# Optimization experiments

Measured on AMD Instinct MI355X. Metric: run time of the kernel, lower is better.

## Reference

```python
import jax, jax.numpy as jnp
import numpy as np

B = 65536
DIM = 8
HIS_LEN = 5
KIND_LEN = 10
HIS_ITEM_DIM = (1 + KIND_LEN) * DIM  # 88
ALL_DIM = DIM * (5 + KIND_LEN) + HIS_ITEM_DIM  # 208


def _linear_params(key, in_dim, out_dim):
    k1, k2 = jax.random.split(key)
    bound = 1.0 / np.sqrt(in_dim)
    w = jax.random.uniform(k1, (out_dim, in_dim), jnp.float32, -bound, bound)
    b = jax.random.uniform(k2, (out_dim,), jnp.float32, -bound, bound)
    return w, b


def setup_inputs() -> dict:
    key = jax.random.key(0)
    ks = jax.random.split(key, 20)
    inp = {
        'userid': jax.random.randint(ks[0], (B, 1), 0, 1000000),
        'itemid': jax.random.randint(ks[1], (B, 1), 0, 1000000),
        'user_age': jax.random.randint(ks[2], (B, 1), 0, 8),
        'gender': jax.random.randint(ks[3], (B, 1), 0, 3),
        'user_occupation': jax.random.randint(ks[4], (B, 1), 0, 25),
        'item_kind': jax.random.randint(ks[5], (B, KIND_LEN), 0, 20),
        'item_id_his': jax.random.randint(ks[6], (B, HIS_LEN), 0, 1000000),
        'item_kind_his': jax.random.randint(ks[7], (B, HIS_LEN, KIND_LEN), 0, 20),
        'user_emb': jax.random.normal(ks[8], (1000000, DIM), jnp.float32),
        'item_emb': jax.random.normal(ks[9], (1000000, DIM), jnp.float32),
        'age_emb': jax.random.normal(ks[10], (8, DIM), jnp.float32),
        'gender_emb': jax.random.normal(ks[11], (3, DIM), jnp.float32),
        'occ_emb': jax.random.normal(ks[12], (25, DIM), jnp.float32),
        'kind_emb': jax.random.normal(ks[13], (20, DIM), jnp.float32),
    }
    act_dims = [(HIS_ITEM_DIM * 3, 64), (64, 32), (32, 1)]
    for i, (di, do) in enumerate(act_dims, 1):
        w, b = _linear_params(jax.random.fold_in(key, 100 + i), di, do)
        inp[f'act_w{i}'], inp[f'act_b{i}'] = w, b
    mlp_dims = [(ALL_DIM, 128), (128, 64), (64, 32), (32, 1)]
    for i, (di, do) in enumerate(mlp_dims, 1):
        w, b = _linear_params(jax.random.fold_in(key, 200 + i), di, do)
        inp[f'mlp_w{i}'], inp[f'mlp_b{i}'] = w, b
    return inp


def _forward(userid, itemid, user_age, gender, user_occupation, item_kind,
             item_id_his, item_kind_his, user_emb, item_emb, age_emb,
             gender_emb, occ_emb, kind_emb,
             act_w1, act_b1, act_w2, act_b2, act_w3, act_b3,
             mlp_w1, mlp_b1, mlp_w2, mlp_b2, mlp_w3, mlp_b3, mlp_w4, mlp_b4):
    b = userid.shape[0]
    user_w = user_emb[userid]          # [b,1,8]
    item_w = item_emb[itemid]          # [b,1,8]
    age_w = age_emb[user_age]          # [b,1,8]
    gen_w = gender_emb[gender]         # [b,1,8]
    occ_w = occ_emb[user_occupation]   # [b,1,8]
    kind_w = kind_emb[item_kind]       # [b,10,8]
    kind_w = kind_w * (item_kind != 0)[..., None].astype(kind_w.dtype)

    # history: vectorized over his_len
    his_item_w = item_emb[item_id_his]           # [b,5,8]
    his_kind_w = kind_emb[item_kind_his]         # [b,5,10,8]
    his_kind_w = his_kind_w * (item_kind_his != 0)[..., None].astype(his_kind_w.dtype)
    his_feature = jnp.concatenate([his_item_w[:, :, None, :], his_kind_w], axis=2)
    his_feature = his_feature.reshape(b, HIS_LEN, HIS_ITEM_DIM)  # [b,5,88]

    item_feat_now = jnp.concatenate([item_w, kind_w], axis=1).reshape(b, 1, HIS_ITEM_DIM)
    item_feat_now = jnp.broadcast_to(item_feat_now, (b, HIS_LEN, HIS_ITEM_DIM))

    # ActUnit: i_in = [i1, i1-i2, i2]; score = MLP(i_in); act_weight = i1 * score
    i1, i2 = his_feature, item_feat_now
    i_in = jnp.concatenate([i1, i1 - i2, i2], axis=-1)  # [b,5,264]
    h = jax.nn.relu(jnp.einsum('bsd,od->bso', i_in, act_w1) + act_b1)
    h = jax.nn.relu(jnp.einsum('bsd,od->bso', h, act_w2) + act_b2)
    score = jnp.einsum('bsd,od->bso', h, act_w3) + act_b3  # [b,5,1]
    act_weight = i1 * score
    his_pool = jnp.sum(his_feature * act_weight, axis=1)  # [b,88]

    all_feat = jnp.concatenate([user_w, item_w, age_w, gen_w, occ_w, kind_w], axis=1).reshape(b, -1)
    all_feat = jnp.concatenate([all_feat, his_pool], axis=-1)  # [b,208]

    h = jax.nn.relu(all_feat @ mlp_w1.T + mlp_b1)
    h = jax.nn.relu(h @ mlp_w2.T + mlp_b2)
    h = jax.nn.relu(h @ mlp_w3.T + mlp_b3)
    logit = h @ mlp_w4.T + mlp_b4  # [b,1]
    return jax.nn.sigmoid(logit)


def reference(userid, itemid, user_age, gender, user_occupation, item_kind,
              item_id_his, item_kind_his, user_emb, item_emb, age_emb,
              gender_emb, occ_emb, kind_emb,
              act_w1, act_b1, act_w2, act_b2, act_w3, act_b3,
              mlp_w1, mlp_b1, mlp_w2, mlp_b2, mlp_w3, mlp_b3, mlp_w4, mlp_b4):
    return _forward(userid, itemid, user_age, gender, user_occupation, item_kind,
                    item_id_his, item_kind_his, user_emb, item_emb, age_emb,
                    gender_emb, occ_emb, kind_emb,
                    act_w1, act_b1, act_w2, act_b2, act_w3, act_b3,
                    mlp_w1, mlp_b1, mlp_w2, mlp_b2, mlp_w3, mlp_b3, mlp_w4, mlp_b4)
```

## Files before the change

### kernel.cpp

```cpp
#include <hip/hip_runtime.h>
#include <cstdint>
#include <math.h>

#define BATCH    65536
#define HIS_LEN  5
#define KIND_LEN 10
#define SB       64
#define NTH      256

typedef float    v2f __attribute__((ext_vector_type(2)));
typedef float    v4f __attribute__((ext_vector_type(4)));
typedef _Float16 v2h __attribute__((ext_vector_type(2)));
typedef _Float16 v8h __attribute__((ext_vector_type(8)));
__device__ __forceinline__ v2f mk2(float a, float b){ v2f r; r.x=a; r.y=b; return r; }
#define C2H(u)  __builtin_bit_cast(v2h,(unsigned)(u))
#define C8H(u4) __builtin_bit_cast(v8h,(u4))

#if __has_builtin(__builtin_amdgcn_fdot2)
__device__ __forceinline__ float FD2(v2h a, v2h b, float c){
  return __builtin_amdgcn_fdot2(a, b, c, false);
}
#else
__device__ __forceinline__ float FD2(v2h a, v2h b, float c){
  return c + (float)a.x*(float)b.x + (float)a.y*(float)b.y;
}
#endif

__device__ __forceinline__ unsigned short f2h(float f){
  return __builtin_bit_cast(unsigned short, (_Float16)f);
}
__device__ __forceinline__ unsigned pack2h(float a, float b){
  return (unsigned)f2h(a) | ((unsigned)f2h(b) << 16);
}
__device__ __forceinline__ v2h pkh(float a, float b){
  return __builtin_bit_cast(v2h, __builtin_amdgcn_cvt_pkrtz(a, b));
}

#define OFF_WC1H 0
#define OFF_AB1  6144
#define OFF_W2H  6208
#define OFF_AB2  7232
#define OFF_W3   7264
#define OFF_AB3  7296
#define OFF_MB2  7297
#define OFF_MB3  7361
#define OFF_M4   7393
#define OFF_MB4  7425
#define OFF_M3H  7428
#define OFF_W1F  8452
#define OFF_MB1  22788
#define OFF_W2F  22916
#define PREP_N   27012
#define W1F4  2113
#define W2F4  5729
#define M3H4  1857

#define TPF   6144
#define M3HL  1856
#define PFF   8704
#define W2HF4 2192
#define MB1F  9986
#define H2F4  1088
#define LDSF  10114

typedef const float* fp;

__device__ __forceinline__ float m1s_val(fp m1, int o, int q, int t){
  if(t >= 52) return 0.f;
  int src;
  if(t<8){ int E = (q==0)?0:(8+8*q); src = E + t; }
  else if(t<30){ int d=t-8; int idx = 8*(d>>1)+2*q+(d&1);
                 src = (idx<8) ? (8+idx) : (32+idx); }
  else { int d=t-30; int idx = 8*(d>>1)+2*q+(d&1); src = 120+idx; }
  return m1[o*208 + src];
}
__device__ __forceinline__ float m1k(fp m1, int o, int k){
  return m1s_val(m1, o, k/56, k%56);
}
__device__ __forceinline__ float w1c_val(fp aw1, int o, int q, int h, int d){
  if(d >= 22) return 0.f;
  int idx = 8*(d>>1) + 2*q + (d&1);
  return h ? (aw1[o*264+176+idx] - aw1[o*264+88+idx])
           : (aw1[o*264+idx]     + aw1[o*264+88+idx]);
}

__global__ void din_prep(fp aw1, fp ab1, fp aw2, fp ab2, fp aw3, fp ab3,
                         fp m1,  fp mb1, fp m2,  fp mb2, fp m3,  fp mb3,
                         fp m4,  fp mb4, float* __restrict__ ws){
  int j = blockIdx.x*blockDim.x + threadIdx.x;
  unsigned* wsu = (unsigned*)ws;
  if(j < 6144){
    int h = j/3072, r = j%3072;
    int slot = r/12, dw = r - slot*12;
    int o = slot>>2, q = slot&3;
    wsu[OFF_WC1H + j] = pack2h(w1c_val(aw1,o,q,h,2*dw), w1c_val(aw1,o,q,h,2*dw+1));
    return;
  } j -= 6144;
  if(j < 64){ ws[OFF_AB1 + j] = ab1[j]; return; } j -= 64;
  if(j < 1024){
    int pp = j>>5, q = (j>>3)&3, dw = j&7;
    int o = 8*q + dw;
    wsu[OFF_W2H + j] = pack2h(aw2[o*64 + 2*pp], aw2[o*64 + 2*pp+1]);
    return;
  } j -= 1024;
  if(j < 32){ ws[OFF_AB2 + j] = ab2[j]; return; } j -= 32;
  if(j < 32){ ws[OFF_W3  + j] = aw3[j]; return; } j -= 32;
  if(j < 1){ ws[OFF_AB3] = ab3[0]; return; } j -= 1;
  if(j < 64){ ws[OFF_MB2 + j] = mb2[j]; return; } j -= 64;
  if(j < 32){ ws[OFF_MB3 + j] = mb3[j]; return; } j -= 32;
  if(j < 32){ ws[OFF_M4  + j] = m4[j];  return; } j -= 32;
  if(j < 1){ ws[OFF_MB4] = mb4[0]; return; } j -= 1;
  if(j < 2){ ws[7426 + j] = 0.f; return; } j -= 2;
  if(j < 1024){
    int qq = j>>8, rr = j&255, ip = rr>>5, dw = rr&31;
    wsu[OFF_M3H + j] = pack2h(m3[dw*64 + 16*qq + 2*ip], m3[dw*64 + 16*qq + 2*ip+1]);
    return;
  } j -= 1024;
  if(j < 14336){
    int frag = j>>2, jr = j&3;
    int lane = frag & 63, nt = frag >> 6;
    int n = nt/7, t = nt - 7*n;
    int o = 16*n + (lane&15);
    int k0 = t*32 + ((lane>>4)<<3) + 2*jr;
    wsu[OFF_W1F + j] = pack2h(m1k(m1,o,k0), m1k(m1,o,k0+1));
    return;
  } j -= 14336;
  if(j < 128){ ws[OFF_MB1 + j] = mb1[j]; return; } j -= 128;
  if(j < 4096){
    int frag = j>>2, jr = j&3;
    int lane = frag & 63, nt = frag >> 6;
    int n2 = nt>>2, t2 = nt&3;
    int o = 16*n2 + (lane&15);
    int k0 = t2*32 + ((lane>>4)<<3) + 2*jr;
    wsu[OFF_W2F + j] = pack2h(m2[o*128 + k0], m2[o*128 + k0+1]);
    return;
  }
}

template<int CTL>
__device__ __forceinline__ float qp(float v){
  return __uint_as_float((unsigned)__builtin_amdgcn_update_dpp(
      0, (int)__float_as_uint(v), CTL, 0xF, 0xF, true));
}
__device__ __forceinline__ float bsum4(float v){
  v += qp<0xB1>(v);
  v += qp<0x4E>(v);
  return v;
}

__device__ __forceinline__ void ldst16(void* l, const void* g){
  __builtin_amdgcn_global_load_lds(
      (const __attribute__((address_space(1))) unsigned int*)(uintptr_t)g,
      (__attribute__((address_space(3))) unsigned int*)(uintptr_t)l, 16, 0, 0);
}
__device__ __forceinline__ void ldst4(void* l, const void* g){
  __builtin_amdgcn_global_load_lds(
      (const __attribute__((address_space(1))) unsigned int*)(uintptr_t)g,
      (__attribute__((address_space(3))) unsigned int*)(uintptr_t)l, 4, 0, 0);
}

__device__ __forceinline__ void gather_h(const float2* __restrict__ itemp,
                                         const float2* __restrict__ kindp,
                                         int item_idx, const int* __restrict__ kidx,
                                         int q, v2h* f){
  float2 v = itemp[item_idx*4 + q];
  f[0] = pkh(v.x, v.y);
  #pragma unroll
  for(int r=0;r<KIND_LEN;r++){
    int ki = kidx[r];
    float2 w = kindp[ki*4 + q];
    float mx = ki ? w.x : 0.f, my = ki ? w.y : 0.f;
    f[1+r] = pkh(mx, my);
  }
}

template<int NS>
__device__ __forceinline__ void hist_pass(int b, int s0, int q, int wid,
    const float2* __restrict__ item_emb, const float2* __restrict__ kind_emb,
    const int* __restrict__ his_id, const int* __restrict__ his_kind,
    const float* ls, const float4* ls4, const unsigned* tpu, v2f* poolv){
  v2h i1h[NS][11];
  #pragma unroll
  for(int t=0;t<NS;t++)
    gather_h(item_emb, kind_emb, his_id[b*HIS_LEN + s0 + t],
             his_kind + (b*HIS_LEN + s0 + t)*KIND_LEN, q, i1h[t]);
  float h2s[NS][8];
  #pragma unroll
  for(int t=0;t<NS;t++)
    #pragma unroll
    for(int k=0;k<8;k++) h2s[t][k] = 0.f;

  #pragma unroll 1
  for(int p=0;p<32;p++){
    const uint4* wr0 = (const uint4*)(ls4 + ((2*p  )*4+q)*3);
    const uint4* wr1 = (const uint4*)(ls4 + ((2*p+1)*4+q)*3);
    uint4 r0=wr0[0], r1=wr0[1], r2=wr0[2];
    uint4 s0v=wr1[0], s1v=wr1[1], s2v=wr1[2];
    unsigned w0[12] = {r0.x,r0.y,r0.z,r0.w, r1.x,r1.y,r1.z,r1.w, r2.x,r2.y,r2.z,r2.w};
    unsigned w1[12] = {s0v.x,s0v.y,s0v.z,s0v.w, s1v.x,s1v.y,s1v.z,s1v.w, s2v.x,s2v.y,s2v.z,s2v.w};
    v2h t2 = C2H(tpu[p*SB + wid]);
    v2h hpv[NS];
    #pragma unroll
    for(int t=0;t<NS;t++){
      float aA=0.f, aB=0.f, cA=0.f, cB=0.f;
      #pragma unroll
      for(int u=0;u<11;u++){
        if(u&1){ aB = FD2(C2H(w0[u]), i1h[t][u], aB); cB = FD2(C2H(w1[u]), i1h[t][u], cB); }
        else   { aA = FD2(C2H(w0[u]), i1h[t][u], aA); cA = FD2(C2H(w1[u]), i1h[t][u], cA); }
      }
      float h0 = fmaxf(bsum4(aA+aB) + (float)t2.x, 0.f);
      float h1 = fmaxf(bsum4(cA+cB) + (float)t2.y, 0.f);
      hpv[t] = pkh(h0, h1);
    }
    uint4 wa = *(const uint4*)(ls4 + W2HF4 + (p*4+q)*2);
    uint4 wb = *(const uint4*)(ls4 + W2HF4 + (p*4+q)*2 + 1);
    unsigned w2d[8] = {wa.x,wa.y,wa.z,wa.w, wb.x,wb.y,wb.z,wb.w};
    #pragma unroll
    for(int t=0;t<NS;t++)
      #pragma unroll
      for(int k=0;k<8;k++) h2s[t][k] = FD2(C2H(w2d[k]), hpv[t], h2s[t][k]);
  }
  #pragma unroll
  for(int t=0;t<NS;t++){
    float scp = 0.f;
    #pragma unroll
    for(int j=0;j<8;j++){
      float hx = fmaxf(h2s[t][j] + ls[PFF+1088+8*q+j], 0.f);
      scp += ls[PFF+1120+8*q+j]*hx;
    }
    float sc = bsum4(scp) + ls[PFF+1152];
    #pragma unroll
    for(int j=0;j<11;j++){
      float sx = (float)i1h[t][j].x, sy = (float)i1h[t][j].y;
      poolv[j] = __builtin_elementwise_fma(mk2(sx*sc, sy*sc), mk2(sx, sy), poolv[j]);
    }
  }
}

__global__ void __launch_bounds__(NTH, 4)
din_main(const int* __restrict__ userid, const int* __restrict__ itemid,
         const int* __restrict__ age,    const int* __restrict__ gen,
         const int* __restrict__ occ,    const int* __restrict__ item_kind,
         const int* __restrict__ his_id, const int* __restrict__ his_kind,
         const float2* __restrict__ user_emb, const float2* __restrict__ item_emb,
         const float2* __restrict__ age_emb,  const float2* __restrict__ gen_emb,
         const float2* __restrict__ occ_emb,  const float2* __restrict__ kind_emb,
         const float* __restrict__ ws, float* __restrict__ out){
  const int tid  = threadIdx.x;
  const int q    = tid & 3;
  const int sl   = (tid & 63) >> 2;
  const int wv   = __builtin_amdgcn_readfirstlane(tid >> 6);
  const int wid  = wv*16 + sl;
  const int b    = blockIdx.x*SB + wid;
  const int l    = tid & 63;
  const int sA   = wv*16 + (l&15);
  const int kb   = l >> 4;

  __shared__ __align__(16) float ls[LDSF];
  float4* ls4 = (float4*)ls;
  const float* wsc = ws;
  const float4* ws4 = (const float4*)ws;
  const uint4* wsu4 = (const uint4*)ws;
  unsigned* tpu = (unsigned*)(ls + TPF);

  #pragma unroll
  for(int k=0;k<5;k++){ int j = k*NTH + tid; ldst4(ls + PFF + j, wsc + OFF_AB1 + j); }
  { int j = 5*NTH + tid;
    if(j < 1282) ldst4(ls + PFF + j, wsc + OFF_AB1 + j); }
  if(tid < 128) ldst4(ls + MB1F + tid, wsc + OFF_MB1 + tid);
  #pragma unroll
  for(int k=0;k<6;k++){ int j = k*NTH + tid; ldst16(ls4 + j, ws4 + j); }

  v2h i2h[11];
  gather_h(item_emb, kind_emb, itemid[b], item_kind + b*KIND_LEN, q, i2h);

  __syncthreads();

  #pragma unroll 1
  for(int p=0;p<32;p++){
    const uint4* wr0 = (const uint4*)(ls4 + 768 + ((2*p  )*4+q)*3);
    const uint4* wr1 = (const uint4*)(ls4 + 768 + ((2*p+1)*4+q)*3);
    uint4 r0=wr0[0], r1=wr0[1], r2=wr0[2];
    uint4 s0v=wr1[0], s1v=wr1[1], s2v=wr1[2];
    unsigned w0[12] = {r0.x,r0.y,r0.z,r0.w, r1.x,r1.y,r1.z,r1.w, r2.x,r2.y,r2.z,r2.w};
    unsigned w1[12] = {s0v.x,s0v.y,s0v.z,s0v.w, s1v.x,s1v.y,s1v.z,s1v.w, s2v.x,s2v.y,s2v.z,s2v.w};
    float aA=0.f, aB=0.f, cA=0.f, cB=0.f;
    #pragma unroll
    for(int u=0;u<11;u++){
      if(u&1){ aB = FD2(C2H(w0[u]), i2h[u], aB); cB = FD2(C2H(w1[u]), i2h[u], cB); }
      else   { aA = FD2(C2H(w0[u]), i2h[u], aA); cA = FD2(C2H(w1[u]), i2h[u], cA); }
    }
    float sA2 = bsum4(aA+aB), sB2 = bsum4(cA+cB);
    if(q==0){
      float2 bb = ((const float2*)(ls+PFF))[p];
      tpu[p*SB + wid] = __builtin_bit_cast(unsigned, pkh(sA2+bb.x, sB2+bb.y));
    }
  }
  __syncthreads();

  v2f poolv[11];
  #pragma unroll
  for(int d=0;d<11;d++) poolv[d]=mk2(0.f,0.f);
  hist_pass<2>(b, 0, q, wid, item_emb, kind_emb, his_id, his_kind, ls, ls4, tpu, poolv);
  hist_pass<2>(b, 2, q, wid, item_emb, kind_emb, his_id, his_kind, ls, ls4, tpu, poolv);
  hist_pass<1>(b, 4, q, wid, item_emb, kind_emb, his_id, his_kind, ls, ls4, tpu, poolv);

  gather_h(item_emb, kind_emb, itemid[b], item_kind + b*KIND_LEN, q, i2h);
  v2h fe[26];
  {
    const float2* ep = (q==0)? user_emb : (q==1)? age_emb : (q==2)? gen_emb : occ_emb;
    int ei = (q==0)? userid[b] : (q==1)? age[b] : (q==2)? gen[b] : occ[b];
    #pragma unroll
    for(int k=0;k<4;k++){ float2 v = ep[ei*4+k]; fe[k] = pkh(v.x, v.y); }
  }
  #pragma unroll
  for(int j=0;j<11;j++) fe[4+j]  = i2h[j];
  #pragma unroll
  for(int j=0;j<11;j++) fe[15+j] = pkh(poolv[j].x, poolv[j].y);

  __syncthreads();

  {
    unsigned xd[28];
    #pragma unroll
    for(int u=0;u<26;u++) xd[u] = __builtin_bit_cast(unsigned, fe[u]);
    xd[26] = 0; xd[27] = 0;
    uint4* xp = (uint4*)(ls4 + wid*29 + q*7);
    #pragma unroll
    for(int ct=0; ct<7; ct++){
      uint4 t; t.x=xd[4*ct]; t.y=xd[4*ct+1]; t.z=xd[4*ct+2]; t.w=xd[4*ct+3];
      xp[ct] = t;
    }
  }
  __syncthreads();

  uint4 af[7];
  #pragma unroll
  for(int t=0;t<7;t++) af[t] = *(const uint4*)(ls4 + sA*29 + t*4 + kb);

  ldst16(ls4 + M3HL + (tid>>6)*66 + (tid&63), ws4 + M3H4 + tid);

  __syncthreads();

  v4f acc1[8];
  #pragma unroll
  for(int n=0;n<8;n++){
    float bb = ls[MB1F + n*16 + (l&15)];
    v4f c = {bb, bb, bb, bb};
    #pragma unroll
    for(int t=0;t<7;t++){
      uint4 bw = wsu4[W1F4 + (n*7+t)*64 + l];
      c = __builtin_amdgcn_mfma_f32_16x16x32_f16(C8H(af[t]), C8H(bw), c, 0, 0, 0);
    }
    acc1[n] = c;
  }
  {
    _Float16* h1p = (_Float16*)ls;
    #pragma unroll
    for(int n=0;n<8;n++)
      #pragma unroll
      for(int i=0;i<4;i++)
        h1p[(wv*16 + kb*4 + i)*136 + 16*n + (l&15)] =
            (_Float16)fmaxf(acc1[n][i], 0.f);
  }
  __syncthreads();

  v4f acc2[4];
  #pragma unroll
  for(int n2=0;n2<4;n2++){
    float bb = ls[PFF+1153 + n2*16 + (l&15)];
    v4f c = {bb, bb, bb, bb};
    acc2[n2] = c;
  }
  #pragma unroll
  for(int t2=0;t2<4;t2++){
    uint4 aw = *(const uint4*)(ls4 + sA*17 + t2*4 + kb);
    #pragma unroll
    for(int n2=0;n2<4;n2++){
      uint4 bw = wsu4[W2F4 + (n2*4+t2)*64 + l];
      acc2[n2] = __builtin_amdgcn_mfma_f32_16x16x32_f16(C8H(aw), C8H(bw), acc2[n2], 0, 0, 0);
    }
  }
  {
    _Float16* h2p = (_Float16*)(ls4 + H2F4);
    #pragma unroll
    for(int n2=0;n2<4;n2++)
      #pragma unroll
      for(int i=0;i<4;i++)
        h2p[(wv*16 + kb*4 + i)*72 + 16*n2 + (l&15)] =
            (_Float16)fmaxf(acc2[n2][i], 0.f);
  }
  __syncthreads();

  v2h hp3[8];
  {
    const uint4* hr = (const uint4*)(ls4 + H2F4 + wid*9 + 2*q);
    uint4 d0 = hr[0], d1 = hr[1];
    hp3[0]=C2H(d0.x); hp3[1]=C2H(d0.y); hp3[2]=C2H(d0.z); hp3[3]=C2H(d0.w);
    hp3[4]=C2H(d1.x); hp3[5]=C2H(d1.y); hp3[6]=C2H(d1.z); hp3[7]=C2H(d1.w);
  }
  float x = ls[PFF+1281];
  #pragma unroll
  for(int g=0;g<4;g++){
    float a[8];
    #pragma unroll
    for(int j=0;j<8;j++) a[j]=0.f;
    #pragma unroll
    for(int ip=0;ip<8;ip++){
      const uint4* w3p = (const uint4*)(ls4 + M3HL + q*66 + ip*8 + 2*g);
      uint4 b0=w3p[0], b1=w3p[1];
      a[0]=FD2(C2H(b0.x),hp3[ip],a[0]); a[1]=FD2(C2H(b0.y),hp3[ip],a[1]);
      a[2]=FD2(C2H(b0.z),hp3[ip],a[2]); a[3]=FD2(C2H(b0.w),hp3[ip],a[3]);
      a[4]=FD2(C2H(b1.x),hp3[ip],a[4]); a[5]=FD2(C2H(b1.y),hp3[ip],a[5]);
      a[6]=FD2(C2H(b1.z),hp3[ip],a[6]); a[7]=FD2(C2H(b1.w),hp3[ip],a[7]);
    }
    #pragma unroll
    for(int j=0;j<8;j++) a[j] = bsum4(a[j]);
    #pragma unroll
    for(int j=0;j<8;j++)
      x += ls[PFF+1249+8*g+j] * fmaxf(a[j] + ls[PFF+1217+8*g+j], 0.f);
  }

  if(q==0) out[b] = 1.0f/(1.0f + __expf(-x));
}

extern "C" void kernel_launch(void* const* d_in, const int* in_sizes, int n_in,
                              void* d_out, int out_size, void* d_ws, size_t ws_size,
                              hipStream_t stream){
  const int* userid    = (const int*)d_in[0];
  const int* itemid    = (const int*)d_in[1];
  const int* age       = (const int*)d_in[2];
  const int* gen       = (const int*)d_in[3];
  const int* occ       = (const int*)d_in[4];
  const int* item_kind = (const int*)d_in[5];
  const int* his_id    = (const int*)d_in[6];
  const int* his_kind  = (const int*)d_in[7];
  const float2* user_emb = (const float2*)d_in[8];
  const float2* item_emb = (const float2*)d_in[9];
  const float2* age_emb  = (const float2*)d_in[10];
  const float2* gen_emb  = (const float2*)d_in[11];
  const float2* occ_emb  = (const float2*)d_in[12];
  const float2* kind_emb = (const float2*)d_in[13];
  float* ws = (float*)d_ws;

  din_prep<<<(PREP_N+255)/256, 256, 0, stream>>>(
      (fp)d_in[14], (fp)d_in[15], (fp)d_in[16], (fp)d_in[17], (fp)d_in[18], (fp)d_in[19],
      (fp)d_in[20], (fp)d_in[21], (fp)d_in[22], (fp)d_in[23], (fp)d_in[24], (fp)d_in[25],
      (fp)d_in[26], (fp)d_in[27], ws);

  din_main<<<BATCH/SB, NTH, 0, stream>>>(
      userid, itemid, age, gen, occ, item_kind, his_id, his_kind,
      user_emb, item_emb, age_emb, gen_emb, occ_emb, kind_emb,
      ws, (float*)d_out);
}
```

Baseline: 242.2 us.

## Compute attention MLP with MFMA per history step, prefetching next gather

Replaces the fdot2-based attention MLP (a per-sample target projection pass plus hist_pass loops over history items) with per-history-step MFMA matmuls. Each step feeds the concatenated history and target features into a 16x16x32 f16 MFMA for layer 1 and another MFMA for layer 2, then does a scalar layer 3 and accumulates the pooled result. The next history item's embedding gather is issued before the current step's matmuls so memory latency overlaps compute. The extra LDS this needs forces the launch-bounds occupancy hint down from 4 to 3 blocks, and each step adds three block barriers.

```diff
diff --git a/kernel.cpp b/kernel.cpp
--- a/kernel.cpp
+++ b/kernel.cpp
@@ -36,32 +36,34 @@
   return __builtin_bit_cast(v2h, __builtin_amdgcn_cvt_pkrtz(a, b));
 }
 
-#define OFF_WC1H 0
-#define OFF_AB1  6144
-#define OFF_W2H  6208
-#define OFF_AB2  7232
-#define OFF_W3   7264
-#define OFF_AB3  7296
-#define OFF_MB2  7297
-#define OFF_MB3  7361
-#define OFF_M4   7393
-#define OFF_MB4  7425
+#define OFF_HW1F 0
+#define OFF_AW2F 6144
+#define OFF_PF   7168
 #define OFF_M3H  7428
-#define OFF_W1F  8452
+#define OFF_MW1F 8452
 #define OFF_MB1  22788
-#define OFF_W2F  22916
+#define OFF_MW2F 22916
 #define PREP_N   27012
-#define W1F4  2113
-#define W2F4  5729
+#define AW2F4 1536
 #define M3H4  1857
-
-#define TPF   6144
-#define M3HL  1856
-#define PFF   8704
-#define W2HF4 2192
-#define MB1F  9986
-#define H2F4  1088
-#define LDSF  10114
+#define MW1F4 2113
+#define MW2F4 5729
+
+#define X2B   0
+#define X1B   832
+#define H1B   1664
+#define H2B   2240
+#define M3HL  2816
+#define LAB1  12312
+#define LAB2  12376
+#define LW3   12408
+#define LAB3  12440
+#define LMB2  12441
+#define LMB3  12505
+#define LM4   12537
+#define LMB4  12569
+#define MB1F  12572
+#define LDSF  12700
 
 typedef const float* fp;
 
@@ -83,6 +85,12 @@
   return h ? (aw1[o*264+176+idx] - aw1[o*264+88+idx])
            : (aw1[o*264+idx]     + aw1[o*264+88+idx]);
 }
+__device__ __forceinline__ float hw1v(fp aw1, int o, int k){
+  int h = (k >= 96) ? 1 : 0;
+  int kk = k - 96*h;
+  int q = kk/24, d = kk%24;
+  return (d<22) ? w1c_val(aw1,o,q,h,d) : 0.f;
+}
 
 __global__ void din_prep(fp aw1, fp ab1, fp aw2, fp ab2, fp aw3, fp ab3,
                          fp m1,  fp mb1, fp m2,  fp mb2, fp m3,  fp mb3,
@@ -90,27 +98,36 @@
   int j = blockIdx.x*blockDim.x + threadIdx.x;
   unsigned* wsu = (unsigned*)ws;
   if(j < 6144){
-    int h = j/3072, r = j%3072;
-    int slot = r/12, dw = r - slot*12;
-    int o = slot>>2, q = slot&3;
-    wsu[OFF_WC1H + j] = pack2h(w1c_val(aw1,o,q,h,2*dw), w1c_val(aw1,o,q,h,2*dw+1));
+    int frag = j>>2, jr = j&3;
+    int lane = frag & 63, nt = frag >> 6;
+    int n = nt/6, t = nt%6;
+    int o = 16*n + (lane&15);
+    int k0 = t*32 + ((lane>>4)<<3) + 2*jr;
+    wsu[OFF_HW1F + j] = pack2h(hw1v(aw1,o,k0), hw1v(aw1,o,k0+1));
     return;
   } j -= 6144;
-  if(j < 64){ ws[OFF_AB1 + j] = ab1[j]; return; } j -= 64;
   if(j < 1024){
-    int pp = j>>5, q = (j>>3)&3, dw = j&7;
-    int o = 8*q + dw;
-    wsu[OFF_W2H + j] = pack2h(aw2[o*64 + 2*pp], aw2[o*64 + 2*pp+1]);
+    int frag = j>>2, jr = j&3;
+    int lane = frag & 63, nt = frag >> 6;
+    int n2 = nt>>1, t2 = nt&1;
+    int o = 16*n2 + (lane&15);
+    int k0 = t2*32 + ((lane>>4)<<3) + 2*jr;
+    wsu[OFF_AW2F + j] = pack2h(aw2[o*64 + k0], aw2[o*64 + k0+1]);
     return;
   } j -= 1024;
-  if(j < 32){ ws[OFF_AB2 + j] = ab2[j]; return; } j -= 32;
-  if(j < 32){ ws[OFF_W3  + j] = aw3[j]; return; } j -= 32;
-  if(j < 1){ ws[OFF_AB3] = ab3[0]; return; } j -= 1;
-  if(j < 64){ ws[OFF_MB2 + j] = mb2[j]; return; } j -= 64;
-  if(j < 32){ ws[OFF_MB3 + j] = mb3[j]; return; } j -= 32;
-  if(j < 32){ ws[OFF_M4  + j] = m4[j];  return; } j -= 32;
-  if(j < 1){ ws[OFF_MB4] = mb4[0]; return; } j -= 1;
-  if(j < 2){ ws[7426 + j] = 0.f; return; } j -= 2;
+  if(j < 258){
+    float v;
+    if(j < 64)       v = ab1[j];
+    else if(j < 96)  v = ab2[j-64];
+    else if(j < 128) v = aw3[j-96];
+    else if(j < 129) v = ab3[0];
+    else if(j < 193) v = mb2[j-129];
+    else if(j < 225) v = mb3[j-193];
+    else if(j < 257) v = m4[j-225];
+    else             v = mb4[0];
+    ws[OFF_PF + j] = v; return;
+  } j -= 258;
+  if(j < 2){ ws[OFF_PF+258+j] = 0.f; return; } j -= 2;
   if(j < 1024){
     int qq = j>>8, rr = j&255, ip = rr>>5, dw = rr&31;
     wsu[OFF_M3H + j] = pack2h(m3[dw*64 + 16*qq + 2*ip], m3[dw*64 + 16*qq + 2*ip+1]);
@@ -122,7 +139,7 @@
     int n = nt/7, t = nt - 7*n;
     int o = 16*n + (lane&15);
     int k0 = t*32 + ((lane>>4)<<3) + 2*jr;
-    wsu[OFF_W1F + j] = pack2h(m1k(m1,o,k0), m1k(m1,o,k0+1));
+    wsu[OFF_MW1F + j] = pack2h(m1k(m1,o,k0), m1k(m1,o,k0+1));
     return;
   } j -= 14336;
   if(j < 128){ ws[OFF_MB1 + j] = mb1[j]; return; } j -= 128;
@@ -132,7 +149,7 @@
     int n2 = nt>>2, t2 = nt&3;
     int o = 16*n2 + (lane&15);
     int k0 = t2*32 + ((lane>>4)<<3) + 2*jr;
-    wsu[OFF_W2F + j] = pack2h(m2[o*128 + k0], m2[o*128 + k0+1]);
+    wsu[OFF_MW2F + j] = pack2h(m2[o*128 + k0], m2[o*128 + k0+1]);
     return;
   }
 }
@@ -174,70 +191,21 @@
   }
 }
 
-template<int NS>
-__device__ __forceinline__ void hist_pass(int b, int s0, int q, int wid,
-    const float2* __restrict__ item_emb, const float2* __restrict__ kind_emb,
-    const int* __restrict__ his_id, const int* __restrict__ his_kind,
-    const float* ls, const float4* ls4, const unsigned* tpu, v2f* poolv){
-  v2h i1h[NS][11];
-  #pragma unroll
-  for(int t=0;t<NS;t++)
-    gather_h(item_emb, kind_emb, his_id[b*HIS_LEN + s0 + t],
-             his_kind + (b*HIS_LEN + s0 + t)*KIND_LEN, q, i1h[t]);
-  float h2s[NS][8];
-  #pragma unroll
-  for(int t=0;t<NS;t++)
-    #pragma unroll
-    for(int k=0;k<8;k++) h2s[t][k] = 0.f;
-
-  #pragma unroll 1
-  for(int p=0;p<32;p++){
-    const uint4* wr0 = (const uint4*)(ls4 + ((2*p  )*4+q)*3);
-    const uint4* wr1 = (const uint4*)(ls4 + ((2*p+1)*4+q)*3);
-    uint4 r0=wr0[0], r1=wr0[1], r2=wr0[2];
-    uint4 s0v=wr1[0], s1v=wr1[1], s2v=wr1[2];
-    unsigned w0[12] = {r0.x,r0.y,r0.z,r0.w, r1.x,r1.y,r1.z,r1.w, r2.x,r2.y,r2.z,r2.w};
-    unsigned w1[12] = {s0v.x,s0v.y,s0v.z,s0v.w, s1v.x,s1v.y,s1v.z,s1v.w, s2v.x,s2v.y,s2v.z,s2v.w};
-    v2h t2 = C2H(tpu[p*SB + wid]);
-    v2h hpv[NS];
-    #pragma unroll
-    for(int t=0;t<NS;t++){
-      float aA=0.f, aB=0.f, cA=0.f, cB=0.f;
-      #pragma unroll
-      for(int u=0;u<11;u++){
-        if(u&1){ aB = FD2(C2H(w0[u]), i1h[t][u], aB); cB = FD2(C2H(w1[u]), i1h[t][u], cB); }
-        else   { aA = FD2(C2H(w0[u]), i1h[t][u], aA); cA = FD2(C2H(w1[u]), i1h[t][u], cA); }
-      }
-      float h0 = fmaxf(bsum4(aA+aB) + (float)t2.x, 0.f);
-      float h1 = fmaxf(bsum4(cA+cB) + (float)t2.y, 0.f);
-      hpv[t] = pkh(h0, h1);
-    }
-    uint4 wa = *(const uint4*)(ls4 + W2HF4 + (p*4+q)*2);
-    uint4 wb = *(const uint4*)(ls4 + W2HF4 + (p*4+q)*2 + 1);
-    unsigned w2d[8] = {wa.x,wa.y,wa.z,wa.w, wb.x,wb.y,wb.z,wb.w};
-    #pragma unroll
-    for(int t=0;t<NS;t++)
-      #pragma unroll
-      for(int k=0;k<8;k++) h2s[t][k] = FD2(C2H(w2d[k]), hpv[t], h2s[t][k]);
-  }
-  #pragma unroll
-  for(int t=0;t<NS;t++){
-    float scp = 0.f;
-    #pragma unroll
-    for(int j=0;j<8;j++){
-      float hx = fmaxf(h2s[t][j] + ls[PFF+1088+8*q+j], 0.f);
-      scp += ls[PFF+1120+8*q+j]*hx;
-    }
-    float sc = bsum4(scp) + ls[PFF+1152];
-    #pragma unroll
-    for(int j=0;j<11;j++){
-      float sx = (float)i1h[t][j].x, sy = (float)i1h[t][j].y;
-      poolv[j] = __builtin_elementwise_fma(mk2(sx*sc, sy*sc), mk2(sx, sy), poolv[j]);
-    }
-  }
-}
-
-__global__ void __launch_bounds__(NTH, 4)
+__device__ __forceinline__ void write_X(float4* ls4, int base, int wid, int q,
+                                        const v2h* f){
+  unsigned xd[12];
+  #pragma unroll
+  for(int r=0;r<11;r++) xd[r] = __builtin_bit_cast(unsigned, f[r]);
+  xd[11] = 0;
+  uint4* xp = (uint4*)(ls4 + base + wid*13 + 3*q);
+  #pragma unroll
+  for(int c=0;c<3;c++){
+    uint4 t; t.x=xd[4*c]; t.y=xd[4*c+1]; t.z=xd[4*c+2]; t.w=xd[4*c+3];
+    xp[c] = t;
+  }
+}
+
+__global__ void __launch_bounds__(NTH, 3)
 din_main(const int* __restrict__ userid, const int* __restrict__ itemid,
          const int* __restrict__ age,    const int* __restrict__ gen,
          const int* __restrict__ occ,    const int* __restrict__ item_kind,
@@ -253,72 +221,119 @@
   const int wid  = wv*16 + sl;
   const int b    = blockIdx.x*SB + wid;
   const int l    = tid & 63;
-  const int sA   = wv*16 + (l&15);
+  const int sr   = wv*16 + (l&15);
   const int kb   = l >> 4;
 
   __shared__ __align__(16) float ls[LDSF];
   float4* ls4 = (float4*)ls;
+  const uint4* lsu4 = (const uint4*)ls;
   const float* wsc = ws;
   const float4* ws4 = (const float4*)ws;
   const uint4* wsu4 = (const uint4*)ws;
-  unsigned* tpu = (unsigned*)(ls + TPF);
-
-  #pragma unroll
-  for(int k=0;k<5;k++){ int j = k*NTH + tid; ldst4(ls + PFF + j, wsc + OFF_AB1 + j); }
-  { int j = 5*NTH + tid;
-    if(j < 1282) ldst4(ls + PFF + j, wsc + OFF_AB1 + j); }
+
+  ldst4(ls + LAB1 + tid, wsc + OFF_PF + tid);
+  if(tid < 2)   ldst4(ls + LAB1 + 256 + tid, wsc + OFF_PF + 256 + tid);
   if(tid < 128) ldst4(ls + MB1F + tid, wsc + OFF_MB1 + tid);
-  #pragma unroll
-  for(int k=0;k<6;k++){ int j = k*NTH + tid; ldst16(ls4 + j, ws4 + j); }
-
+  ldst16(ls4 + M3HL + (tid>>6)*66 + (tid&63), ws4 + M3H4 + tid);
+
+  {
+    v2h i2t[11];
+    gather_h(item_emb, kind_emb, itemid[b], item_kind + b*KIND_LEN, q, i2t);
+    write_X(ls4, X2B, wid, q, i2t);
+  }
+  v2h i1c[11], i1n[11];
+  gather_h(item_emb, kind_emb, his_id[b*HIS_LEN], his_kind + b*HIS_LEN*KIND_LEN,
+           q, i1c);
+
+  v2f poolv[11];
+  #pragma unroll
+  for(int d=0;d<11;d++) poolv[d]=mk2(0.f,0.f);
   v2h i2h[11];
-  gather_h(item_emb, kind_emb, itemid[b], item_kind + b*KIND_LEN, q, i2h);
+  float2 exr[4];
 
   __syncthreads();
 
   #pragma unroll 1
-  for(int p=0;p<32;p++){
-    const uint4* wr0 = (const uint4*)(ls4 + 768 + ((2*p  )*4+q)*3);
-    const uint4* wr1 = (const uint4*)(ls4 + 768 + ((2*p+1)*4+q)*3);
-    uint4 r0=wr0[0], r1=wr0[1], r2=wr0[2];
-    uint4 s0v=wr1[0], s1v=wr1[1], s2v=wr1[2];
-    unsigned w0[12] = {r0.x,r0.y,r0.z,r0.w, r1.x,r1.y,r1.z,r1.w, r2.x,r2.y,r2.z,r2.w};
-    unsigned w1[12] = {s0v.x,s0v.y,s0v.z,s0v.w, s1v.x,s1v.y,s1v.z,s1v.w, s2v.x,s2v.y,s2v.z,s2v.w};
-    float aA=0.f, aB=0.f, cA=0.f, cB=0.f;
-    #pragma unroll
-    for(int u=0;u<11;u++){
-      if(u&1){ aB = FD2(C2H(w0[u]), i2h[u], aB); cB = FD2(C2H(w1[u]), i2h[u], cB); }
-      else   { aA = FD2(C2H(w0[u]), i2h[u], aA); cA = FD2(C2H(w1[u]), i2h[u], cA); }
-    }
-    float sA2 = bsum4(aA+aB), sB2 = bsum4(cA+cB);
-    if(q==0){
-      float2 bb = ((const float2*)(ls+PFF))[p];
-      tpu[p*SB + wid] = __builtin_bit_cast(unsigned, pkh(sA2+bb.x, sB2+bb.y));
-    }
-  }
-  __syncthreads();
-
-  v2f poolv[11];
-  #pragma unroll
-  for(int d=0;d<11;d++) poolv[d]=mk2(0.f,0.f);
-  hist_pass<2>(b, 0, q, wid, item_emb, kind_emb, his_id, his_kind, ls, ls4, tpu, poolv);
-  hist_pass<2>(b, 2, q, wid, item_emb, kind_emb, his_id, his_kind, ls, ls4, tpu, poolv);
-  hist_pass<1>(b, 4, q, wid, item_emb, kind_emb, his_id, his_kind, ls, ls4, tpu, poolv);
-
-  gather_h(item_emb, kind_emb, itemid[b], item_kind + b*KIND_LEN, q, i2h);
+  for(int s=0;s<5;s++){
+    write_X(ls4, X1B, wid, q, i1c);
+    __syncthreads();
+    if(s < 4){
+      gather_h(item_emb, kind_emb, his_id[b*HIS_LEN+s+1],
+               his_kind + (b*HIS_LEN+s+1)*KIND_LEN, q, i1n);
+    } else {
+      gather_h(item_emb, kind_emb, itemid[b], item_kind + b*KIND_LEN, q, i2h);
+      const float2* ep = (q==0)? user_emb : (q==1)? age_emb : (q==2)? gen_emb : occ_emb;
+      int ei = (q==0)? userid[b] : (q==1)? age[b] : (q==2)? gen[b] : occ[b];
+      #pragma unroll
+      for(int k=0;k<4;k++) exr[k] = ep[ei*4+k];
+    }
+    {
+      uint4 a1[6];
+      #pragma unroll
+      for(int t=0;t<3;t++) a1[t]   = lsu4[X2B*0 + X1B + sr*13 + 4*t + kb];
+      #pragma unroll
+      for(int t=0;t<3;t++) a1[3+t] = lsu4[X2B + sr*13 + 4*t + kb];
+      _Float16* h1p = (_Float16*)(ls4 + H1B);
+      #pragma unroll
+      for(int n=0;n<4;n++){
+        float bb = ls[LAB1 + 16*n + (l&15)];
+        v4f c = {bb,bb,bb,bb};
+        #pragma unroll
+        for(int t=0;t<6;t++){
+          uint4 bw = wsu4[(n*6+t)*64 + l];
+          c = __builtin_amdgcn_mfma_f32_16x16x32_f16(C8H(a1[t]), C8H(bw), c, 0, 0, 0);
+        }
+        #pragma unroll
+        for(int i=0;i<4;i++)
+          h1p[(16*wv + 4*kb + i)*72 + 16*n + (l&15)] = (_Float16)fmaxf(c[i],0.f);
+      }
+    }
+    __syncthreads();
+    {
+      uint4 a2[2];
+      #pragma unroll
+      for(int t=0;t<2;t++) a2[t] = lsu4[H1B + sr*9 + 4*t + kb];
+      float* h2p = (float*)(ls4 + H2B);
+      #pragma unroll
+      for(int n2=0;n2<2;n2++){
+        float bb = ls[LAB2 + 16*n2 + (l&15)];
+        v4f c = {bb,bb,bb,bb};
+        #pragma unroll
+        for(int t=0;t<2;t++){
+          uint4 bw = wsu4[AW2F4 + (n2*2+t)*64 + l];
+          c = __builtin_amdgcn_mfma_f32_16x16x32_f16(C8H(a2[t]), C8H(bw), c, 0, 0, 0);
+        }
+        #pragma unroll
+        for(int i=0;i<4;i++)
+          h2p[(16*wv + 4*kb + i)*36 + 16*n2 + (l&15)] = fmaxf(c[i],0.f);
+      }
+    }
+    __syncthreads();
+    {
+      const float4* hr = (const float4*)(ls4 + H2B + wid*9 + 2*q);
+      float4 h0 = hr[0], h1v = hr[1];
+      float scp = h0.x*ls[LW3+8*q]   + h0.y*ls[LW3+8*q+1]
+                + h0.z*ls[LW3+8*q+2] + h0.w*ls[LW3+8*q+3]
+                + h1v.x*ls[LW3+8*q+4] + h1v.y*ls[LW3+8*q+5]
+                + h1v.z*ls[LW3+8*q+6] + h1v.w*ls[LW3+8*q+7];
+      float sc = bsum4(scp) + ls[LAB3];
+      #pragma unroll
+      for(int j=0;j<11;j++){
+        float sx = (float)i1c[j].x, sy = (float)i1c[j].y;
+        poolv[j] = __builtin_elementwise_fma(mk2(sx*sc, sy*sc), mk2(sx, sy), poolv[j]);
+      }
+    }
+    #pragma unroll
+    for(int j=0;j<11;j++) i1c[j] = i1n[j];
+  }
+
   v2h fe[26];
-  {
-    const float2* ep = (q==0)? user_emb : (q==1)? age_emb : (q==2)? gen_emb : occ_emb;
-    int ei = (q==0)? userid[b] : (q==1)? age[b] : (q==2)? gen[b] : occ[b];
-    #pragma unroll
-    for(int k=0;k<4;k++){ float2 v = ep[ei*4+k]; fe[k] = pkh(v.x, v.y); }
-  }
+  #pragma unroll
+  for(int k=0;k<4;k++) fe[k] = pkh(exr[k].x, exr[k].y);
   #pragma unroll
   for(int j=0;j<11;j++) fe[4+j]  = i2h[j];
   #pragma unroll
   for(int j=0;j<11;j++) fe[15+j] = pkh(poolv[j].x, poolv[j].y);
-
-  __syncthreads();
 
   {
     unsigned xd[28];
@@ -336,10 +351,7 @@
 
   uint4 af[7];
   #pragma unroll
-  for(int t=0;t<7;t++) af[t] = *(const uint4*)(ls4 + sA*29 + t*4 + kb);
-
-  ldst16(ls4 + M3HL + (tid>>6)*66 + (tid&63), ws4 + M3H4 + tid);
-
+  for(int t=0;t<7;t++) af[t] = lsu4[sr*29 + t*4 + kb];
   __syncthreads();
 
   v4f acc1[8];
@@ -349,7 +361,7 @@
     v4f c = {bb, bb, bb, bb};
     #pragma unroll
     for(int t=0;t<7;t++){
-      uint4 bw = wsu4[W1F4 + (n*7+t)*64 + l];
+      uint4 bw = wsu4[MW1F4 + (n*7+t)*64 + l];
       c = __builtin_amdgcn_mfma_f32_16x16x32_f16(C8H(af[t]), C8H(bw), c, 0, 0, 0);
     }
     acc1[n] = c;
@@ -360,7 +372,7 @@
     for(int n=0;n<8;n++)
       #pragma unroll
       for(int i=0;i<4;i++)
-        h1p[(wv*16 + kb*4 + i)*136 + 16*n + (l&15)] =
+        h1p[(16*wv + 4*kb + i)*136 + 16*n + (l&15)] =
             (_Float16)fmaxf(acc1[n][i], 0.f);
   }
   __syncthreads();
@@ -368,38 +380,38 @@
   v4f acc2[4];
   #pragma unroll
   for(int n2=0;n2<4;n2++){
-    float bb = ls[PFF+1153 + n2*16 + (l&15)];
+    float bb = ls[LMB2 + n2*16 + (l&15)];
     v4f c = {bb, bb, bb, bb};
     acc2[n2] = c;
   }
   #pragma unroll
   for(int t2=0;t2<4;t2++){
-    uint4 aw = *(const uint4*)(ls4 + sA*17 + t2*4 + kb);
+    uint4 aw = lsu4[sr*17 + t2*4 + kb];
     #pragma unroll
     for(int n2=0;n2<4;n2++){
-      uint4 bw = wsu4[W2F4 + (n2*4+t2)*64 + l];
+      uint4 bw = wsu4[MW2F4 + (n2*4+t2)*64 + l];
       acc2[n2] = __builtin_amdgcn_mfma_f32_16x16x32_f16(C8H(aw), C8H(bw), acc2[n2], 0, 0, 0);
     }
   }
   {
-    _Float16* h2p = (_Float16*)(ls4 + H2F4);
+    _Float16* h2p = (_Float16*)(ls4 + 1088);
     #pragma unroll
     for(int n2=0;n2<4;n2++)
       #pragma unroll
       for(int i=0;i<4;i++)
-        h2p[(wv*16 + kb*4 + i)*72 + 16*n2 + (l&15)] =
+        h2p[(16*wv + 4*kb + i)*72 + 16*n2 + (l&15)] =
             (_Float16)fmaxf(acc2[n2][i], 0.f);
   }
   __syncthreads();
 
   v2h hp3[8];
   {
-    const uint4* hr = (const uint4*)(ls4 + H2F4 + wid*9 + 2*q);
+    const uint4* hr = (const uint4*)(ls4 + 1088 + wid*9 + 2*q);
     uint4 d0 = hr[0], d1 = hr[1];
     hp3[0]=C2H(d0.x); hp3[1]=C2H(d0.y); hp3[2]=C2H(d0.z); hp3[3]=C2H(d0.w);
     hp3[4]=C2H(d1.x); hp3[5]=C2H(d1.y); hp3[6]=C2H(d1.z); hp3[7]=C2H(d1.w);
   }
-  float x = ls[PFF+1281];
+  float x = ls[LMB4];
   #pragma unroll
   for(int g=0;g<4;g++){
     float a[8];
@@ -418,7 +430,7 @@
     for(int j=0;j<8;j++) a[j] = bsum4(a[j]);
     #pragma unroll
     for(int j=0;j<8;j++)
-      x += ls[PFF+1249+8*g+j] * fmaxf(a[j] + ls[PFF+1217+8*g+j], 0.f);
+      x += ls[LM4+8*g+j] * fmaxf(a[j] + ls[LMB3+8*g+j], 0.f);
   }
 
   if(q==0) out[b] = 1.0f/(1.0f + __expf(-x));
```

Result: no change. 238.1 us (-1.7%).
